# Kernel tuning notes

Hardware: AMD Instinct MI355X
Metric: run time of the kernel (lower is better)

## Reference

```python
import jax, jax.numpy as jnp
import numpy as np

BSZ, SL, K, D_IN, D_OUT = 2, 1024, 24, 512, 512
K_U, K_Y = 3, 2
USE_HANKEL_L = False


def get_top_eigh(l, k, use_hankel_L):
    i = np.arange(1, l + 1, dtype=np.float64)
    s = i[:, None] + i[None, :]
    if use_hankel_L:
        Z = ((-1.0) ** (s - 2.0) + 1.0) * 8.0 / ((s + 3.0) * (s - 1.0) * (s + 1.0))
    else:
        Z = 2.0 / (s ** 3 - s)
    sigma, phi = np.linalg.eigh(Z)  # ascending
    return jnp.asarray(sigma[-k:], jnp.float32), jnp.asarray(phi[:, -k:], jnp.float32)


def shift(x, k):
    # causal shift along time axis 1, zero-padded at the front
    if k == 0:
        return x
    return jnp.pad(x, ((0, 0), (k, 0), (0, 0)))[:, : x.shape[1]]


def fft_causal_conv(filters, u):
    # filters: (l, k); u: (b, l, d) -> (b, l, k, d) causal convolution per filter
    l = u.shape[1]
    n = 2 * l
    F = jnp.fft.rfft(filters, n=n, axis=0)  # (n//2+1, k)
    U = jnp.fft.rfft(u, n=n, axis=1)        # (b, n//2+1, d)
    Y = jnp.fft.irfft(U[:, :, None, :] * F[None, :, :, None], n=n, axis=1)
    return Y[:, :l].astype(u.dtype)


def compute_ar_u(M_u, u):
    # ar_u[b,t,o] = sum_{i<k_u} M_u[i] @ u_{t-i}
    U = jnp.stack([shift(u, i) for i in range(M_u.shape[0])])  # (k_u, b, l, d_in)
    return jnp.einsum('koi,kbli->blo', M_u, U)


def compute_spectral(u, sigma, phi, M_phi_plus, M_phi_minus, m_y):
    l = u.shape[1]
    phi_s = phi * sigma ** 0.25  # eigenvalue-scaled spectral filters (l, k)
    U_plus = fft_causal_conv(phi_s, u)  # (b, l, k, d_in)
    spec = jnp.einsum('blki,koi->blo', U_plus, M_phi_plus)
    if not USE_HANKEL_L:
        # negative-featurization branch: filters modulated by (-1)^i
        alt = ((-1.0) ** jnp.arange(l)).astype(u.dtype)
        U_minus = fft_causal_conv(phi_s * alt[:, None], u)
        spec = spec + jnp.einsum('blki,koi->blo', U_minus, M_phi_minus)
    if m_y is not None:
        spec = shift(spec, m_y.shape[0])  # spectral features enter at lag k_y (paper: t-2)
    return spec


def compute_ar_y(m_y, y):
    # true short linear recurrence on outputs:
    # yhat_t = y_t + sum_{i=1}^{k_y} m_y[i-1] @ yhat_{t-i}; returns the correction term
    k_y, d_out = m_y.shape[0], m_y.shape[1]
    b = y.shape[0]

    def step(carry, y_t):  # carry: (k_y, b, d_out) = [yhat_{t-1}, ..., yhat_{t-k_y}]
        ar_t = jnp.einsum('koj,kbj->bo', m_y, carry)
        yhat_t = y_t + ar_t
        carry = jnp.concatenate([yhat_t[None], carry[:-1]], axis=0)
        return carry, ar_t

    y_tl = jnp.swapaxes(y, 0, 1)  # (l, b, d_out)
    _, ar = jax.lax.scan(step, jnp.zeros((k_y, b, d_out), y.dtype), y_tl)
    return jnp.swapaxes(ar, 0, 1)


def setup_inputs() -> dict:
    key = jax.random.key(0)
    k0, k1, k2, k3, k4 = jax.random.split(key, 5)
    inputs = jax.random.normal(k0, (BSZ, SL, D_IN), jnp.float32)
    M_u = jax.random.normal(k1, (K_U, D_OUT, D_IN), jnp.float32) * 0.02
    M_phi_plus = jax.random.normal(k2, (K, D_OUT, D_IN), jnp.float32) * 0.02
    M_phi_minus = jax.random.normal(k3, (K, D_OUT, D_IN), jnp.float32) * 0.02
    m_y = jax.random.normal(k4, (K_Y, D_OUT, D_OUT), jnp.float32) * 0.02
    sigma, phi = get_top_eigh(SL, K, USE_HANKEL_L)
    return {'inputs': inputs, 'M_u': M_u, 'M_phi_plus': M_phi_plus,
            'M_phi_minus': M_phi_minus, 'm_y': m_y, 'sigma': sigma, 'phi': phi}


def reference(inputs, M_u, M_phi_plus, M_phi_minus, m_y, sigma, phi):
    ar_u = compute_ar_u(M_u, inputs)
    spectral = compute_spectral(inputs, sigma, phi, M_phi_plus, M_phi_minus, m_y)
    y_t = ar_u + spectral
    y_t = y_t + compute_ar_y(m_y, y_t)  # learnable_m_y=True branch
    return y_t  # dropout p=0.0 (identity)
```

## Files before the change

### kernel.cpp

```cpp
#include <hip/hip_runtime.h>
#include <hip/hip_bf16.h>


typedef unsigned short u16;
typedef __attribute__((ext_vector_type(8))) short  vshort8;
typedef __attribute__((ext_vector_type(4))) short  vshort4;
typedef __attribute__((ext_vector_type(4))) float  f32x4;
typedef __attribute__((ext_vector_type(4))) unsigned int vuint4;

__device__ __forceinline__ u16 f2b(float x) {
  __hip_bfloat16 h = __float2bfloat16(x);
  return __builtin_bit_cast(u16, h);
}
__device__ __forceinline__ float b2f(u16 x) {
  unsigned int u = ((unsigned int)x) << 16;
  return __builtin_bit_cast(float, u);
}

__device__ __forceinline__ void gll16(const u16* g, u16* l) {
  __builtin_amdgcn_global_load_lds((__attribute__((address_space(1))) void*)g,
                                   (__attribute__((address_space(3))) void*)l,
                                   16, 0, 0);
}

struct GB {
  const u16* A; const u16* B;
  float* Cf; u16* Cb;
  const float* zf; float* out;
  u16* A2T; u16* Au;
  const u16* zp;
  int M, N;
};

template<int V>
__global__ __launch_bounds__(256) void g2(GB a) {
  const int tid = threadIdx.x;
  int bn = blockIdx.x, bm = blockIdx.y;
  int zz = blockIdx.z;
  int cj = 0, cb = 0, cd = 0, slot = 0;
  int kbeg = 0, kend = 0;
  if (V == 0) {
    int f = blockIdx.x;
    int o = (f & 7) * 408 + (f >> 3);
    bm = o & 15; bn = o >> 4; kend = 512;
  }
  if (V == 1) {
    int f = blockIdx.x;
    int o = (f & 7) * 144 + (f >> 3);
    const int offs1[8] = {0, 256, 480, 672, 832, 960, 1056, 1120};
    cj = 0;
    if (o >= offs1[1]) cj = 1;
    if (o >= offs1[2]) cj = 2;
    if (o >= offs1[3]) cj = 3;
    if (o >= offs1[4]) cj = 4;
    if (o >= offs1[5]) cj = 5;
    if (o >= offs1[6]) cj = 6;
    if (o >= offs1[7]) cj = 7;
    int r = o - offs1[cj];
    int run = 8 - cj;
    int combo = r / run;
    bm = cj + (r - combo * run);
    int zzc = combo >> 2; bn = combo & 3;
    cb = zzc & 1; cd = bm - cj;
    slot = zzc * 8 + cj;
    kbeg = (zzc >> 1) * 1536; kend = kbeg + 1536;
  }
  if (V == 2) {
    int f = blockIdx.x;
    int o = (f & 7) * 68 + (f >> 3);
    const int offs2[16] = {0, 64, 124, 180, 232, 280, 324, 364,
                           400, 432, 460, 484, 504, 520, 532, 540};
    int s = 0;
#pragma unroll
    for (int c = 1; c < 16; ++c)
      if (o >= offs2[c]) s = c;
    int r = o - offs2[s];
    bm = s + (r >> 2); bn = r & 3;
    zz = s;
    kbeg = s * 1024; kend = kbeg + 1024;
  }
  const int m0 = bm * 128, n0 = bn * 128;
  if (V == 3 || V == 5 || V == 6 || V == 7) kend = 1024;

  __shared__ u16 lA[2][4096], lB[2][4096];
  f32x4 acc[4][4];
#pragma unroll
  for (int i = 0; i < 4; i++)
#pragma unroll
    for (int j = 0; j < 4; j++) acc[i][j] = f32x4{0.f, 0.f, 0.f, 0.f};

  const int lane = tid & 63, wv = tid >> 6, wr = wv >> 1, wc = wv & 1;
  const u16* Ap = a.A;
  if (V == 5) Ap = a.A + (size_t)zz * 524288;
  const u16* zpl = a.zp + lane * 8;

  auto gaddrA = [&](int it, int k0) -> const u16* {
    int lrow = (it * 4 + wv) * 16 + (lane & 15);
    int kk = k0 + ((lane >> 4) << 3);
    if (V == 0) return Ap + (size_t)(m0 + lrow) * 512 + kk;
    if (V == 1) return Ap + (size_t)cd * 786432 + (size_t)lrow * 6144 + kk;
    if (V == 2) {
      int m = m0 + lrow, j = m >> 6, b = (m >> 5) & 1, c = m & 31;
      int tau = kk >> 9, p = kk & 511;
      if (tau > j) return zpl;
      return Ap + (size_t)(b * 1024 + c * 32 + j - tau) * 512 + p;
    }
    if (V == 3) { int m = m0 + lrow; return (m < a.M) ? Ap + (size_t)m * 1024 + kk : zpl; }
    if (V == 5) return Ap + (size_t)(m0 + lrow) * 1024 + kk;
    if (V == 6) return (lrow < 64) ? Ap + (size_t)lrow * 1024 + kk : zpl;
    if (lrow < 32) {
      int b = lrow & 1, k2 = lrow >> 1;
      return Ap + (size_t)(b * 32 + 2 * k2) * 1024 + kk;
    }
    return zpl;
  };
  auto gaddrB = [&](int it, int k0) -> const u16* {
    int lrow = (it * 4 + wv) * 16 + (lane & 15);
    int kk = k0 + ((lane >> 4) << 3);
    int n = n0 + lrow;
    if (V == 0) return a.B + (size_t)n * 512 + kk;
    if (V == 1) {
      int kh = kk >> 7, sp = kk & 127;
      return a.B + (size_t)(cb * 512 + n) * 49152 + kh * 1024 + cj * 128 + sp;
    }
    if (V == 2) {
      int tau = kk >> 9, p = kk & 511;
      return a.B + (size_t)tau * 524288 + (size_t)n * 1024 + p;
    }
    if (V == 3) {
      int jn = n >> 9, o = n & 511;
      return a.B + (size_t)(jn + 1) * 524288 + (size_t)o * 1024 + kk;
    }
    if (V == 5) return a.B + (size_t)n * 1024 + kk;
    return (n < 512)
        ? a.B + (size_t)32 * 524288 + (size_t)n * 1024 + kk
        : a.B + (size_t)31 * 524288 + (size_t)(n - 512) * 1024 + kk;
  };

  auto stage = [&](int c, int k0) {
#pragma unroll
    for (int it = 0; it < 2; ++it) {
      int weff = wv + it * 4;
      gll16(gaddrA(it, k0), &lA[c][weff * 512]);
      gll16(gaddrB(it, k0), &lB[c][weff * 512]);
    }
  };

  if (kbeg < kend) stage(0, kbeg);
  __syncthreads();
  int cur = 0;
  for (int k0 = kbeg; k0 < kend; k0 += 32) {
    if (k0 + 32 < kend) stage(cur ^ 1, k0 + 32);
    vshort8 af[4], bf_[4];
#pragma unroll
    for (int s = 0; s < 4; s++) {
      af[s]  = *(const vshort8*)&lA[cur][(((wr * 4 + s) * 4 + (lane >> 4)) * 16 + (lane & 15)) * 8];
      bf_[s] = *(const vshort8*)&lB[cur][(((wc * 4 + s) * 4 + (lane >> 4)) * 16 + (lane & 15)) * 8];
    }
#pragma unroll
    for (int i = 0; i < 4; i++)
#pragma unroll
      for (int j = 0; j < 4; j++)
        acc[i][j] = __builtin_amdgcn_mfma_f32_16x16x32_bf16(af[i], bf_[j], acc[i][j], 0, 0, 0);
    __syncthreads();
    cur ^= 1;
  }

#pragma unroll
  for (int i = 0; i < 4; i++) {
    int em = m0 + wr * 64 + i * 16 + ((lane >> 4) << 2);
#pragma unroll
    for (int j = 0; j < 4; j++) {
      int n = n0 + wc * 64 + j * 16 + (lane & 15);
      f32x4 v = acc[i][j];
      if (V == 0) {
        int b = em >> 10, s = em & 1023;
        if (n < 24576) {
          int kh = n >> 9, o = n & 511;
          vshort4 pk = { (short)f2b(v[0]), (short)f2b(v[1]), (short)f2b(v[2]), (short)f2b(v[3]) };
          *(vshort4*)(&a.A2T[(size_t)(b * 512 + o) * 49152 + (size_t)kh * 1024 + s]) = pk;
        } else {
          int jj = (n - 24576) >> 9, o = n & 511;
#pragma unroll
          for (int t = 0; t < 4; t++)
            a.Au[((size_t)(b * 3 + jj) * 1024 + (s + t)) * 512 + o] = f2b(v[t]);
        }
      } else if (V == 1) {
        u16* C = a.Cb + (size_t)slot * 524288;
#pragma unroll
        for (int t = 0; t < 4; t++) C[(size_t)(em + t) * 512 + n] = f2b(v[t]);
      } else if (V == 2) {
        float* C = a.Cf + (size_t)zz * 1048576;
#pragma unroll
        for (int t = 0; t < 4; t++) C[(size_t)(em + t) * 512 + n] = v[t];
      } else if (V == 3) {
        int jj = n >> 9, oo = n & 511;
#pragma unroll
        for (int t = 0; t < 4; t++) {
          int m = em + t;
          if (m < a.M) {
            int b = m >> 5, c = m & 31;
            float zv = a.zf[(size_t)(jj * 64 + b * 32 + c) * 512 + oo];
            a.out[(size_t)b * 524288 + (size_t)(c * 32 + jj) * 512 + oo] = v[t] + zv;
          }
        }
      } else if (V == 5) {
        u16* C = a.Cb + (size_t)zz * 524288;
#pragma unroll
        for (int t = 0; t < 4; t++) C[(size_t)(em + t) * 1024 + n] = f2b(v[t]);
      } else if (V == 6) {
        int jrow = (n < 512) ? 31 : 30, oo = n & 511;
#pragma unroll
        for (int t = 0; t < 4; t++) {
          int m = em + t;
          if (m < 62) {
            int b = m & 1, c = m >> 1;
            a.Cf[(size_t)m * 1024 + n] =
                v[t] + a.zf[(size_t)(jrow * 64 + b * 32 + (c + 1)) * 512 + oo];
          }
        }
      } else {
        int jrow = (n < 512) ? 31 : 30, oo = n & 511;
#pragma unroll
        for (int t = 0; t < 4; t++) {
          int m = em + t;
          if (m < 32) {
            int b = m & 1, k2 = m >> 1;
            float val = v[t] + a.zf[(size_t)(jrow * 64 + b * 32 + 2 * k2) * 512 + oo];
            a.Cb[(size_t)(b * 32 + 2 * k2 + 1) * 1024 + n] = f2b(val);
          }
        }
      }
    }
  }
}

__global__ void k_prep_X(const float* __restrict__ u, u16* __restrict__ X, int n) {
  int i = blockIdx.x * 256 + threadIdx.x;
  if (i < n) X[i] = f2b(u[i]);
}

__global__ void k_prep_phis(const float* __restrict__ phi, const float* __restrict__ sigma,
                            float* __restrict__ phis) {
  int i = blockIdx.x * 256 + threadIdx.x;
  if (i >= 1024 * 48) return;
  int tau = i / 48, kf = i % 48, k = (kf >= 24) ? kf - 24 : kf;
  float v = phi[tau * 24 + k] * powf(sigma[k], 0.25f);
  if (kf >= 24 && (tau & 1)) v = -v;
  phis[i] = v;
}

__global__ void k_prep_W1(const float* __restrict__ Mp, const float* __restrict__ Mm,
                          const float* __restrict__ Mu, u16* __restrict__ W1) {
  int i = blockIdx.x * 256 + threadIdx.x;
  if (i >= 13369344) return;
  float v;
  if (i < 6291456) v = Mp[i];
  else if (i < 12582912) v = Mm[i - 6291456];
  else v = Mu[i - 12582912];
  W1[i] = f2b(v);
}

__global__ void k_prep_Wtoep(const float* __restrict__ phis, u16* __restrict__ W) {
  int i = blockIdx.x * 256 + threadIdx.x;
  if (i >= 6291456) return;
  int kap = i % 6144, row = i / 6144;
  int tp = row & 127, d = row >> 7;
  int kh = kap >> 7, sp = kap & 127;
  int tau = d * 128 + tp - sp;
  W[i] = (tau >= 0 && tau < 1024) ? f2b(phis[tau * 48 + kh]) : (u16)0;
}

__global__ void k_initTop(const float* __restrict__ my, u16* __restrict__ Top) {
  int i = blockIdx.x * 256 + threadIdx.x;
  if (i >= 1048576) return;
  int mat = i >> 19, rem = i & 524287, o = rem >> 10, k = rem & 1023;
  u16 v;
  if (mat == 0) v = (k == o) ? (u16)0x3F80 : (u16)0;
  else v = (k < 512) ? f2b(my[o * 512 + k]) : f2b(my[262144 + o * 512 + (k - 512)]);
  Top[i] = v;
}

__global__ __launch_bounds__(256) void k_transT(const u16* __restrict__ Top,
                                                u16* __restrict__ STc, int c) {
  __shared__ u16 tile[64][72];
  int tx = blockIdx.x, ty = blockIdx.y;
  int tid = threadIdx.x;
  int r = tid >> 2, seg = tid & 3;
  int k = ty * 64 + r;
  const u16* src = (k < 512) ? Top + (size_t)c * 524288 + (size_t)k * 1024 + tx * 64
                             : Top + (size_t)(c - 1) * 524288 + (size_t)(k - 512) * 1024 + tx * 64;
  *(vuint4*)&tile[r][seg * 16]     = *(const vuint4*)(src + seg * 16);
  *(vuint4*)&tile[r][seg * 16 + 8] = *(const vuint4*)(src + seg * 16 + 8);
  __syncthreads();
  int n = tx * 64 + r;
  u16 tmp[16];
#pragma unroll
  for (int j = 0; j < 16; j++) tmp[j] = tile[seg * 16 + j][r];
  *(vuint4*)&STc[(size_t)n * 1024 + ty * 64 + seg * 16]     = *(vuint4*)&tmp[0];
  *(vuint4*)&STc[(size_t)n * 1024 + ty * 64 + seg * 16 + 8] = *(vuint4*)&tmp[8];
}

__device__ __forceinline__ void addp(float* acc, vuint4 v) {
  const unsigned int* vu = (const unsigned int*)&v;
#pragma unroll
  for (int e = 0; e < 4; ++e) {
    unsigned int pw = vu[e];
    acc[2 * e]     += __builtin_bit_cast(float, (pw & 0xffffu) << 16);
    acc[2 * e + 1] += __builtin_bit_cast(float, pw & 0xffff0000u);
  }
}

__global__ void k_combine(const u16* __restrict__ parts, const u16* __restrict__ Au,
                          u16* __restrict__ ybf) {
  int i = blockIdx.x * 256 + threadIdx.x;
  if (i >= 131072) return;
  int og = i & 63, t = (i >> 6) & 1023, b = i >> 16;
  float acc[8];
#pragma unroll
  for (int e = 0; e < 8; ++e) acc[e] = 0.f;
#pragma unroll
  for (int j = 0; j < 3; j++)
    if (t >= j)
      addp(acc, *(const vuint4*)(Au + ((size_t)(b * 3 + j) * 1024 + (t - j)) * 512 + og * 8));
  if (t >= 2) {
    int tp = t - 2, bmv = tp >> 7;
#pragma unroll
    for (int g = 0; g < 8; ++g) {
      if ((g & 1) != b) continue;
      const u16* base = parts + (size_t)(g * 8) * 524288 + (size_t)tp * 512 + og * 8;
      for (int j = 0; j <= bmv; ++j)
        addp(acc, *(const vuint4*)(base + (size_t)j * 524288));
    }
  }
  u16 o16[8];
#pragma unroll
  for (int e = 0; e < 8; ++e) o16[e] = f2b(acc[e]);
  *(vuint4*)(ybf + ((size_t)(b * 1024 + t)) * 512 + og * 8) = *(vuint4*)o16;
}

__global__ void k_zreduce(const float* __restrict__ zp, float* __restrict__ z) {
  int i = blockIdx.x * 256 + threadIdx.x;
  if (i >= 1048576) return;
  int nsum = (i >> 16) + 1;
  float s = 0.f;
  for (int j = 0; j < nsum; ++j) s += zp[(size_t)j * 1048576 + i];
  z[i] = s;
}

__global__ void k_wm(const float* __restrict__ zf, u16* __restrict__ Wm) {
  int i = blockIdx.x * 256 + threadIdx.x;
  if (i >= 65536) return;
  int row = i >> 10, n = i & 1023;
  int b = row & 1, c = row >> 1;
  int jrow = (n < 512) ? 31 : 30, oo = n & 511;
  Wm[i] = f2b(zf[(size_t)(jrow * 64 + b * 32 + c) * 512 + oo]);
}

__global__ __launch_bounds__(256) void k_bnd2(const u16* __restrict__ Top,
                                              const float* __restrict__ ubuf,
                                              float* __restrict__ bnd,
                                              u16* __restrict__ Abnd, int k) {
  __shared__ float st[2048];
  int tid = threadIdx.x;
  const float* s0 = bnd + (size_t)k * 2048;
  for (int j = tid; j < 2048; j += 256) st[j] = s0[j];
  __syncthreads();
  int q4 = blockIdx.x * 256 + tid;
  int q = q4 >> 2, quarter = q4 & 3;
  int b = q >> 10, kk = q & 1023;
  const u16* row = (kk < 512) ? Top + (size_t)64 * 524288 + (size_t)kk * 1024
                              : Top + (size_t)63 * 524288 + (size_t)(kk - 512) * 1024;
  const float* stb = st + b * 1024 + quarter * 256;
  const u16* rp = row + quarter * 256;
  float sum = 0.f;
  for (int t = 0; t < 32; ++t) {
    vuint4 v = *(const vuint4*)(rp + t * 8);
    const unsigned int* vu = (const unsigned int*)&v;
#pragma unroll
    for (int e = 0; e < 4; ++e) {
      unsigned int pw = vu[e];
      float lo = __builtin_bit_cast(float, (pw & 0xffffu) << 16);
      float hi = __builtin_bit_cast(float, pw & 0xffff0000u);
      sum += lo * stb[t * 8 + e * 2] + hi * stb[t * 8 + e * 2 + 1];
    }
  }
  sum += __shfl_xor(sum, 1);
  sum += __shfl_xor(sum, 2);
  if (quarter == 0) {
    float s = sum + ubuf[(size_t)(4 * k + b) * 1024 + kk];
    bnd[(size_t)(k + 1) * 2048 + b * 1024 + kk] = s;
    Abnd[(size_t)(b * 32 + 2 * k + 2) * 1024 + kk] = f2b(s);
  }
}

extern "C" void kernel_launch(void* const* d_in, const int* in_sizes, int n_in,
                              void* d_out, int out_size, void* d_ws, size_t ws_size,
                              hipStream_t stream) {
  const float* u     = (const float*)d_in[0];
  const float* Mu    = (const float*)d_in[1];
  const float* Mp    = (const float*)d_in[2];
  const float* Mm    = (const float*)d_in[3];
  const float* my    = (const float*)d_in[4];
  const float* sigma = (const float*)d_in[5];
  const float* phi   = (const float*)d_in[6];
  float* out = (float*)d_out;

  char* ws = (char*)d_ws;
  size_t off = 0;
  auto alc = [&](size_t b) { size_t p = off; off = (off + b + 255) & ~(size_t)255; return p; };
  u16*  X     = (u16*)(ws + alc(2097152));
  u16*  Wtoep = (u16*)(ws + alc(12582912));
  u16*  A2T   = (u16*)(ws + alc(100663296));
  u16*  Au    = (u16*)(ws + alc(6291456));
  u16*  W1    = (u16*)(ws + alc(26738688));
  char* ptail = ws + alc(40370176); (void)ptail;
  float* phis = (float*)(ws + alc(196608));
  float* bnd  = (float*)(ws + alc(131072));
  u16*  Abnd  = (u16*)(ws + alc(131072));
  u16*  Wm    = (u16*)(ws + alc(131072));
  float* ubuf = (float*)(ws + alc(262144));
  u16*  zpad  = (u16*)(ws + alc(32768));
  if (off > ws_size) return;
  u16*  partsBf = (u16*)W1;
  float* zparts = (float*)W1;
  u16*  ybf = A2T;
  float* zf = (float*)((char*)A2T + (4 << 20));
  u16*  Top = (u16*)((char*)A2T + (size_t)(8 << 20));
  u16*  STc = (u16*)((char*)A2T + (size_t)(76 << 20));

  hipMemsetAsync(zpad, 0, 32768, stream);

  k_prep_X<<<dim3(4096), 256, 0, stream>>>(u, X, 1048576);
  k_prep_phis<<<dim3(192), 256, 0, stream>>>(phi, sigma, phis);
  k_prep_W1<<<dim3(52224), 256, 0, stream>>>(Mp, Mm, Mu, W1);
  k_prep_Wtoep<<<dim3(24576), 256, 0, stream>>>(phis, Wtoep);

  {
    GB g{}; g.A = X; g.B = W1; g.A2T = A2T; g.Au = Au; g.zp = zpad;
    g.M = 2048; g.N = 26112;
    g2<0><<<dim3(3264), 256, 0, stream>>>(g);
  }
  {
    GB g{}; g.A = Wtoep; g.B = A2T; g.Cb = partsBf; g.zp = zpad;
    g.M = 1024; g.N = 512;
    g2<1><<<dim3(1152), 256, 0, stream>>>(g);
  }
  k_combine<<<dim3(512), 256, 0, stream>>>(partsBf, Au, ybf);

  k_initTop<<<dim3(4096), 256, 0, stream>>>(my, Top);
  {
    const int cs[5] = {1, 2, 4, 8, 16};
    for (int li = 0; li < 5; ++li) {
      int c = cs[li];
      k_transT<<<dim3(16, 16), 256, 0, stream>>>(Top, STc, c);
      GB s{}; s.A = Top + 524288; s.B = STc; s.Cb = Top + (size_t)(c + 1) * 524288;
      s.zp = zpad; s.M = 512; s.N = 1024;
      g2<5><<<dim3(8, 4, c), 256, 0, stream>>>(s);
    }
    k_transT<<<dim3(16, 16), 256, 0, stream>>>(Top, STc, 32);
    GB s{}; s.A = Top + (size_t)31 * 524288; s.B = STc;
    s.Cb = Top + (size_t)63 * 524288; s.zp = zpad; s.M = 512; s.N = 1024;
    g2<5><<<dim3(8, 4, 2), 256, 0, stream>>>(s);
  }

  {
    GB g{}; g.A = ybf; g.B = Top; g.Cf = zparts; g.zp = zpad;
    g.M = 2048; g.N = 512;
    g2<2><<<dim3(544), 256, 0, stream>>>(g);
  }
  k_zreduce<<<dim3(4096), 256, 0, stream>>>(zparts, zf);

  k_wm<<<dim3(256), 256, 0, stream>>>(zf, Wm);
  {
    GB g{}; g.A = Wm; g.B = Top; g.Cf = ubuf; g.zf = zf; g.zp = zpad;
    g.M = 64; g.N = 1024;
    g2<6><<<dim3(8, 1, 1), 256, 0, stream>>>(g);
  }
  hipMemsetAsync(bnd, 0, 8192, stream);
  hipMemsetAsync(Abnd, 0, 131072, stream);
  for (int k = 0; k < 15; ++k)
    k_bnd2<<<dim3(32), 256, 0, stream>>>(Top, ubuf, bnd, Abnd, k);
  {
    GB g{}; g.A = Abnd; g.B = Top; g.Cb = Abnd; g.zf = zf; g.zp = zpad;
    g.M = 32; g.N = 1024;
    g2<7><<<dim3(8, 1, 1), 256, 0, stream>>>(g);
  }

  {
    GB g{}; g.A = Abnd; g.B = Top; g.zf = zf; g.out = out; g.zp = zpad;
    g.M = 64; g.N = 16384;
    g2<3><<<dim3(128, 1, 1), 256, 0, stream>>>(g);
  }
}
```

Baseline: 756.9 us.

## Stage V0 GEMM epilogue through LDS for coalesced transposed stores; vectorize prep casts

The V0 GEMM epilogue for the spectral columns now writes bf16 results into shared memory in two passes, transposes them there, and stores 64-byte contiguous runs per row of the transposed A2T buffer. The old path issued scattered 8-byte stores. The shared tiles are merged into one flat buffer so the epilogue can reuse them. Separately, the fp32-to-bf16 prep kernels for X and W1 now process four elements per thread with vector loads and stores. The change adds two extra barriers per block and relies on the block boundaries lining up with the 512-column and 1024-row groupings.

```diff
diff --git a/kernel.cpp b/kernel.cpp
--- a/kernel.cpp
+++ b/kernel.cpp
@@ -82,7 +82,7 @@
   const int m0 = bm * 128, n0 = bn * 128;
   if (V == 3 || V == 5 || V == 6 || V == 7) kend = 1024;
 
-  __shared__ u16 lA[2][4096], lB[2][4096];
+  __shared__ u16 smem[16384];
   f32x4 acc[4][4];
 #pragma unroll
   for (int i = 0; i < 4; i++)
@@ -141,8 +141,8 @@
 #pragma unroll
     for (int it = 0; it < 2; ++it) {
       int weff = wv + it * 4;
-      gll16(gaddrA(it, k0), &lA[c][weff * 512]);
-      gll16(gaddrB(it, k0), &lB[c][weff * 512]);
+      gll16(gaddrA(it, k0), smem + c * 4096 + weff * 512);
+      gll16(gaddrB(it, k0), smem + 8192 + c * 4096 + weff * 512);
     }
   };
 
@@ -154,8 +154,8 @@
     vshort8 af[4], bf_[4];
 #pragma unroll
     for (int s = 0; s < 4; s++) {
-      af[s]  = *(const vshort8*)&lA[cur][(((wr * 4 + s) * 4 + (lane >> 4)) * 16 + (lane & 15)) * 8];
-      bf_[s] = *(const vshort8*)&lB[cur][(((wc * 4 + s) * 4 + (lane >> 4)) * 16 + (lane & 15)) * 8];
+      af[s]  = *(const vshort8*)&smem[cur * 4096 + (((wr * 4 + s) * 4 + (lane >> 4)) * 16 + (lane & 15)) * 8];
+      bf_[s] = *(const vshort8*)&smem[8192 + cur * 4096 + (((wc * 4 + s) * 4 + (lane >> 4)) * 16 + (lane & 15)) * 8];
     }
 #pragma unroll
     for (int i = 0; i < 4; i++)
@@ -164,6 +164,40 @@
         acc[i][j] = __builtin_amdgcn_mfma_f32_16x16x32_bf16(af[i], bf_[j], acc[i][j], 0, 0, 0);
     __syncthreads();
     cur ^= 1;
+  }
+
+  if (V == 0 && bn < 192) {
+    const int strd = 136;
+    const int b = m0 >> 10;
+#pragma unroll
+    for (int p = 0; p < 2; ++p) {
+      __syncthreads();
+#pragma unroll
+      for (int i = 0; i < 4; i++) {
+#pragma unroll
+        for (int jl = 0; jl < 2; jl++) {
+          int j = p * 2 + jl;
+          f32x4 v = acc[i][j];
+          int mloc = wr * 64 + i * 16 + ((lane >> 4) << 2);
+          int phys = (lane & 15) + (jl << 4) + (wc << 5);
+          vshort4 pk = { (short)f2b(v[0]), (short)f2b(v[1]),
+                         (short)f2b(v[2]), (short)f2b(v[3]) };
+          *(vshort4*)&smem[phys * strd + mloc] = pk;
+        }
+      }
+      __syncthreads();
+      int rowp = tid >> 2, t4 = tid & 3;
+      int c15 = rowp & 15, jl = (rowp >> 4) & 1, wcp = rowp >> 5;
+      int n = n0 + wcp * 64 + p * 32 + jl * 16 + c15;
+      int o = n & 511, kh = n >> 9;
+      int sbase = (m0 & 1023) + t4 * 32;
+      u16* dst = a.A2T + (size_t)(b * 512 + o) * 49152 + (size_t)kh * 1024 + sbase;
+      const u16* srcl = &smem[rowp * strd + t4 * 32];
+#pragma unroll
+      for (int q = 0; q < 4; ++q)
+        *(vuint4*)(dst + q * 8) = *(const vuint4*)(srcl + q * 8);
+    }
+    return;
   }
 
 #pragma unroll
@@ -175,16 +209,10 @@
       f32x4 v = acc[i][j];
       if (V == 0) {
         int b = em >> 10, s = em & 1023;
-        if (n < 24576) {
-          int kh = n >> 9, o = n & 511;
-          vshort4 pk = { (short)f2b(v[0]), (short)f2b(v[1]), (short)f2b(v[2]), (short)f2b(v[3]) };
-          *(vshort4*)(&a.A2T[(size_t)(b * 512 + o) * 49152 + (size_t)kh * 1024 + s]) = pk;
-        } else {
-          int jj = (n - 24576) >> 9, o = n & 511;
-#pragma unroll
-          for (int t = 0; t < 4; t++)
-            a.Au[((size_t)(b * 3 + jj) * 1024 + (s + t)) * 512 + o] = f2b(v[t]);
-        }
+        int jj = (n - 24576) >> 9, o = n & 511;
+#pragma unroll
+        for (int t = 0; t < 4; t++)
+          a.Au[((size_t)(b * 3 + jj) * 1024 + (s + t)) * 512 + o] = f2b(v[t]);
       } else if (V == 1) {
         u16* C = a.Cb + (size_t)slot * 524288;
 #pragma unroll
@@ -235,9 +263,12 @@
   }
 }
 
-__global__ void k_prep_X(const float* __restrict__ u, u16* __restrict__ X, int n) {
-  int i = blockIdx.x * 256 + threadIdx.x;
-  if (i < n) X[i] = f2b(u[i]);
+__global__ void k_prep_X(const float* __restrict__ u, u16* __restrict__ X) {
+  int i4 = (blockIdx.x * 256 + threadIdx.x) * 4;
+  if (i4 >= 1048576) return;
+  f32x4 v = *(const f32x4*)(u + i4);
+  vshort4 pk = { (short)f2b(v[0]), (short)f2b(v[1]), (short)f2b(v[2]), (short)f2b(v[3]) };
+  *(vshort4*)(X + i4) = pk;
 }
 
 __global__ void k_prep_phis(const float* __restrict__ phi, const float* __restrict__ sigma,
@@ -252,13 +283,15 @@
 
 __global__ void k_prep_W1(const float* __restrict__ Mp, const float* __restrict__ Mm,
                           const float* __restrict__ Mu, u16* __restrict__ W1) {
-  int i = blockIdx.x * 256 + threadIdx.x;
-  if (i >= 13369344) return;
-  float v;
-  if (i < 6291456) v = Mp[i];
-  else if (i < 12582912) v = Mm[i - 6291456];
-  else v = Mu[i - 12582912];
-  W1[i] = f2b(v);
+  int i4 = (blockIdx.x * 256 + threadIdx.x) * 4;
+  if (i4 >= 13369344) return;
+  const float* src; int off;
+  if (i4 < 6291456) { src = Mp; off = i4; }
+  else if (i4 < 12582912) { src = Mm; off = i4 - 6291456; }
+  else { src = Mu; off = i4 - 12582912; }
+  f32x4 v = *(const f32x4*)(src + off);
+  vshort4 pk = { (short)f2b(v[0]), (short)f2b(v[1]), (short)f2b(v[2]), (short)f2b(v[3]) };
+  *(vshort4*)(W1 + i4) = pk;
 }
 
 __global__ void k_prep_Wtoep(const float* __restrict__ phis, u16* __restrict__ W) {
@@ -431,9 +464,9 @@
 
   hipMemsetAsync(zpad, 0, 32768, stream);
 
-  k_prep_X<<<dim3(4096), 256, 0, stream>>>(u, X, 1048576);
+  k_prep_X<<<dim3(1024), 256, 0, stream>>>(u, X);
   k_prep_phis<<<dim3(192), 256, 0, stream>>>(phi, sigma, phis);
-  k_prep_W1<<<dim3(52224), 256, 0, stream>>>(Mp, Mm, Mu, W1);
+  k_prep_W1<<<dim3(13056), 256, 0, stream>>>(Mp, Mm, Mu, W1);
   k_prep_Wtoep<<<dim3(24576), 256, 0, stream>>>(phis, Wtoep);
 
   {
```

Result: faster. 714.5 us (-5.6%).
